# Kernel tuning notes

Measured on AMD Instinct MI355X. Metric: run time of the kernel, lower is better.

## Reference

```python
import jax, jax.numpy as jnp
import numpy as np

BINS = 2048       # self.bins in HistogramQuant
UPSAMPLE = 128    # self.upsample_rate


def setup_inputs() -> dict:
    key = jax.random.key(0)
    k1, k2 = jax.random.split(key)
    x = jax.random.normal(k1, (64, 1024, 1024), dtype=jnp.float32)
    histogram = jax.random.uniform(k2, (BINS,), dtype=jnp.float32)
    min_val = jnp.zeros((1,), dtype=jnp.float32)
    max_val = jnp.ones((1,), dtype=jnp.float32)
    return {"x": x, "histogram": histogram, "min_val": min_val, "max_val": max_val}


def reference(x, histogram, min_val, max_val):
    # Observer-update branch of HistogramQuant.forward (counter > 0, state
    # initialized). Returns concat([new_histogram(2048), new_min, new_max]).
    xs = jax.lax.stop_gradient(x)  # torch: x = x_orig.detach()
    mn = min_val[0]
    mx = max_val[0]
    cur_min = jnp.min(xs)
    cur_max = jnp.max(xs)
    cmin = jnp.minimum(cur_min, mn)
    cmax0 = jnp.maximum(cur_max, mx)

    # _adjust_min_max
    hbw = (mx - mn) / (BINS * UPSAMPLE)  # fine-grained bin width of old hist
    dr_f = jnp.ceil((cmax0 - cmin) / (BINS * hbw))  # downsample_rate
    cmax = cmax0 + (dr_f * (BINS * hbw) - (cmax0 - cmin))
    start_idx = jnp.round((mn - cmin) / hbw).astype(jnp.int32)

    # torch.histc(x, BINS, min=int(cmin), max=int(cmax)) -- truncated range
    hmn = jnp.trunc(cmin)
    hmx = jnp.trunc(cmax)
    rel = (xs - hmn) / (hmx - hmn)
    idx = jnp.clip(jnp.floor(rel * BINS), 0, BINS - 1).astype(jnp.int32)
    in_range = (xs >= hmn) & (xs <= hmx)  # histc ignores out-of-range values
    hist_new = jax.ops.segment_sum(
        in_range.astype(jnp.float32).ravel(), idx.ravel(), num_segments=BINS)

    # _combine_histograms, done analytically: the torch code upsamples the old
    # histogram by UPSAMPLE, places it at start_idx inside a BINS*dr grid,
    # cumsums, and samples every dr-th entry. The cumsum at grid position p
    # equals (with q = p - start_idx) the inclusive prefix sum of the
    # upsampled old histogram at q, which has closed form
    #   pref[q//U] + (q%U + 1) * old_hist[q//U]
    # so we never materialize the BINS*dr or BINS*U arrays.
    dr = dr_f.astype(jnp.int32)
    pref = jnp.concatenate(
        [jnp.zeros((1,), histogram.dtype), jnp.cumsum(histogram)[:-1]]) * UPSAMPLE
    p = (jnp.arange(BINS, dtype=jnp.int32) + 1) * dr - 1  # sampled positions
    q = p - start_idx
    qc = jnp.clip(q, 0, BINS * UPSAMPLE - 1)
    j = qc // UPSAMPLE
    frac = (qc % UPSAMPLE).astype(histogram.dtype)
    integral = jnp.where(q < 0, 0.0, pref[j] + (frac + 1.0) * histogram[j])
    shifted = jnp.concatenate(
        [jnp.zeros((1,), integral.dtype), integral[:-1]])
    interp = (integral - shifted) / UPSAMPLE

    same = (cmin == mn) & (cmax == mx)
    new_hist = hist_new + jnp.where(same, histogram, interp)
    return jnp.concatenate([new_hist, cmin[None], cmax[None]])
```

## Files before the change

kernel.cpp:

```cpp
#include <hip/hip_runtime.h>
#include <math.h>

#define BINS 2048
#define UPSAMPLE 128

__device__ __forceinline__ unsigned enc_f32(float f) {
    unsigned u = __float_as_uint(f);
    return (u & 0x80000000u) ? ~u : (u | 0x80000000u);
}
__device__ __forceinline__ float dec_f32(unsigned e) {
    unsigned u = (e & 0x80000000u) ? (e ^ 0x80000000u) : ~e;
    return __uint_as_float(u);
}

__global__ void hq_init(float* out) {
    int i = blockIdx.x * blockDim.x + threadIdx.x;
    if (i < BINS) out[i] = 0.0f;
    if (i == BINS)     ((unsigned*)out)[BINS]     = 0xFFFFFFFFu;
    if (i == BINS + 1) ((unsigned*)out)[BINS + 1] = 0u;
}

__global__ void __launch_bounds__(256) hq_minmax(const float4* __restrict__ x4, long n4,
                                                 const float* __restrict__ xt, int ntail,
                                                 unsigned* mm) {
    float vmin = INFINITY, vmax = -INFINITY;
    long i0 = (long)blockIdx.x * blockDim.x + threadIdx.x;
    long stride = (long)gridDim.x * blockDim.x;
    for (long i = i0; i < n4; i += stride) {
        float4 v = x4[i];
        vmin = fminf(vmin, fminf(fminf(v.x, v.y), fminf(v.z, v.w)));
        vmax = fmaxf(vmax, fmaxf(fmaxf(v.x, v.y), fmaxf(v.z, v.w)));
    }
    if (blockIdx.x == 0 && threadIdx.x < ntail) {
        float xv = xt[threadIdx.x];
        vmin = fminf(vmin, xv);
        vmax = fmaxf(vmax, xv);
    }
    #pragma unroll
    for (int off = 32; off; off >>= 1) {
        vmin = fminf(vmin, __shfl_xor(vmin, off));
        vmax = fmaxf(vmax, __shfl_xor(vmax, off));
    }
    __shared__ float smin[4], smax[4];
    int wid = threadIdx.x >> 6, lane = threadIdx.x & 63;
    if (lane == 0) { smin[wid] = vmin; smax[wid] = vmax; }
    __syncthreads();
    if (threadIdx.x == 0) {
        float bmin = fminf(fminf(smin[0], smin[1]), fminf(smin[2], smin[3]));
        float bmax = fmaxf(fmaxf(smax[0], smax[1]), fmaxf(smax[2], smax[3]));
        atomicMin(&mm[0], enc_f32(bmin));
        atomicMax(&mm[1], enc_f32(bmax));
    }
}

__device__ __forceinline__ void hist_bin_add(float xv, float hmn, float hmx, float range,
                                             unsigned* sh) {
    if (xv >= hmn && xv <= hmx) {
        float rel = (xv - hmn) / range;
        int idx = (int)fminf(fmaxf(floorf(rel * (float)BINS), 0.0f), (float)(BINS - 1));
        atomicAdd(&sh[idx], 1u);
    }
}

__global__ void __launch_bounds__(1024) hq_hist(const float4* __restrict__ x4, long n4,
                                                const float* __restrict__ xt, int ntail,
                                                float* __restrict__ out,
                                                const float* __restrict__ min_val,
                                                const float* __restrict__ max_val) {
    __shared__ unsigned sh[BINS];
    for (int i = threadIdx.x; i < BINS; i += blockDim.x) sh[i] = 0u;

    const unsigned* mm = (const unsigned*)(out + BINS);
    float mn = min_val[0], mx = max_val[0];
    float cmin  = fminf(dec_f32(mm[0]), mn);
    float cmax0 = fmaxf(dec_f32(mm[1]), mx);
    float hbw = (mx - mn) / (float)(BINS * UPSAMPLE);
    float bw  = (float)BINS * hbw;
    float dr_f = ceilf((cmax0 - cmin) / bw);
    float cmax = cmax0 + (dr_f * bw - (cmax0 - cmin));
    float hmn = truncf(cmin), hmx = truncf(cmax);
    float range = hmx - hmn;
    __syncthreads();

    long i0 = (long)blockIdx.x * blockDim.x + threadIdx.x;
    long stride = (long)gridDim.x * blockDim.x;
    for (long i = i0; i < n4; i += stride) {
        float4 v = x4[i];
        hist_bin_add(v.x, hmn, hmx, range, sh);
        hist_bin_add(v.y, hmn, hmx, range, sh);
        hist_bin_add(v.z, hmn, hmx, range, sh);
        hist_bin_add(v.w, hmn, hmx, range, sh);
    }
    if (blockIdx.x == 0 && threadIdx.x < ntail) {
        hist_bin_add(xt[threadIdx.x], hmn, hmx, range, sh);
    }
    __syncthreads();
    for (int i = threadIdx.x; i < BINS; i += blockDim.x) {
        unsigned c = sh[i];
        if (c) atomicAdd(&out[i], (float)c);
    }
}

__global__ void __launch_bounds__(1024) hq_finalize(float* __restrict__ out,
                                                    const float* __restrict__ old_hist,
                                                    const float* __restrict__ min_val,
                                                    const float* __restrict__ max_val) {
    __shared__ float h[BINS];
    __shared__ float sc[2][BINS];
    int t = threadIdx.x;

    const unsigned* mm = (const unsigned*)(out + BINS);
    unsigned emin = mm[0], emax = mm[1];
    float mn = min_val[0], mx = max_val[0];

    h[t]        = old_hist[t];
    h[t + 1024] = old_hist[t + 1024];
    sc[0][t]        = h[t];
    sc[0][t + 1024] = h[t + 1024];
    __syncthreads();

    int src = 0;
    for (int off = 1; off < BINS; off <<= 1) {
        int dst = src ^ 1;
        #pragma unroll
        for (int k = 0; k < 2; ++k) {
            int i = t + k * 1024;
            float v = sc[src][i];
            if (i >= off) v += sc[src][i - off];
            sc[dst][i] = v;
        }
        __syncthreads();
        src = dst;
    }
    const float* incl = sc[src];

    float cmin  = fminf(dec_f32(emin), mn);
    float cmax0 = fmaxf(dec_f32(emax), mx);
    float hbw = (mx - mn) / (float)(BINS * UPSAMPLE);
    float bw  = (float)BINS * hbw;
    float dr_f = ceilf((cmax0 - cmin) / bw);
    float cmax = cmax0 + (dr_f * bw - (cmax0 - cmin));
    int dr = (int)dr_f;
    int start_idx = (int)rintf((mn - cmin) / hbw);
    bool same = (cmin == mn) && (cmax == mx);

    #pragma unroll
    for (int k = 0; k < 2; ++k) {
        int i = t + k * 1024;
        float integ_i = 0.0f, integ_p = 0.0f;
        {
            int q = (i + 1) * dr - 1 - start_idx;
            if (q >= 0) {
                int qc = min(q, BINS * UPSAMPLE - 1);
                int j = qc >> 7;
                float pref = (j ? incl[j - 1] : 0.0f) * (float)UPSAMPLE;
                integ_i = pref + ((float)(qc & 127) + 1.0f) * h[j];
            }
        }
        if (i > 0) {
            int q = i * dr - 1 - start_idx;
            if (q >= 0) {
                int qc = min(q, BINS * UPSAMPLE - 1);
                int j = qc >> 7;
                float pref = (j ? incl[j - 1] : 0.0f) * (float)UPSAMPLE;
                integ_p = pref + ((float)(qc & 127) + 1.0f) * h[j];
            }
        }
        float interp = (integ_i - integ_p) * (1.0f / (float)UPSAMPLE);
        out[i] = out[i] + (same ? h[i] : interp);
    }
    if (t == 0) {
        out[BINS]     = cmin;
        out[BINS + 1] = cmax;
    }
}

extern "C" void kernel_launch(void* const* d_in, const int* in_sizes, int n_in,
                              void* d_out, int out_size, void* d_ws, size_t ws_size,
                              hipStream_t stream) {
    (void)d_ws; (void)ws_size; (void)n_in; (void)out_size;
    const float* x         = (const float*)d_in[0];
    const float* histogram = (const float*)d_in[1];
    const float* min_val   = (const float*)d_in[2];
    const float* max_val   = (const float*)d_in[3];
    float* out = (float*)d_out;

    long n  = (long)in_sizes[0];
    long n4 = n >> 2;
    int ntail = (int)(n & 3);
    const float* xt = x + (n4 << 2);

    hq_init<<<(BINS + 2 + 255) / 256, 256, 0, stream>>>(out);
    hq_minmax<<<2048, 256, 0, stream>>>((const float4*)x, n4, xt, ntail,
                                        (unsigned*)(out + BINS));
    hq_hist<<<512, 1024, 0, stream>>>((const float4*)x, n4, xt, ntail, out,
                                      min_val, max_val);
    hq_finalize<<<1, 1024, 0, stream>>>(out, histogram, min_val, max_val);
}
```

Baseline: 436.2 us.

## Fuse min/max and histogram into one pass via fine-grained integer-bin histogram

Replaces the two passes over x (min/max, then histogram) with one pass. That pass bins every value into a fixed fine grid of width 1/2048. Because the histc range endpoints are truncated to integers, each output bin covers a whole number of fine cells, so the final histogram can be rebuilt from fine counts once min/max are known. A 16K-entry shared window holds the common range, with global atomics for outliers. Per-block partials are reduced in a separate kernel. This halves reads of the 256MB input but adds a large workspace, a 4M-entry init, partial writeback, and serial summing in finalize proportional to the range.

```diff
diff --git a/kernel.cpp b/kernel.cpp
--- a/kernel.cpp
+++ b/kernel.cpp
@@ -3,6 +3,16 @@
 
 #define BINS 2048
 #define UPSAMPLE 128
+
+#define LWIN 16384
+#define LHALF 8192
+#define WIDE_N 4194304
+#define WIDE_HALF 2097152
+#define NBLK 512
+#define RGROUPS 8
+
+#define MM_OFF   WIDE_N
+#define PART_OFF (WIDE_N + 16)
 
 __device__ __forceinline__ unsigned enc_f32(float f) {
     unsigned u = __float_as_uint(f);
@@ -13,105 +23,99 @@
     return __uint_as_float(u);
 }
 
-__global__ void hq_init(float* out) {
-    int i = blockIdx.x * blockDim.x + threadIdx.x;
-    if (i < BINS) out[i] = 0.0f;
-    if (i == BINS)     ((unsigned*)out)[BINS]     = 0xFFFFFFFFu;
-    if (i == BINS + 1) ((unsigned*)out)[BINS + 1] = 0u;
-}
-
-__global__ void __launch_bounds__(256) hq_minmax(const float4* __restrict__ x4, long n4,
+__global__ void __launch_bounds__(256) hq_init(unsigned* ws) {
+    long i = (long)blockIdx.x * blockDim.x + threadIdx.x;
+    ((uint4*)ws)[i] = make_uint4(0u, 0u, 0u, 0u);
+    if (i == 0) {
+        ws[MM_OFF]     = 0xFFFFFFFFu;
+        ws[MM_OFF + 1] = 0u;
+    }
+}
+
+__device__ __forceinline__ void fine_add(float c, float& vmin, float& vmax,
+                                         unsigned* sh, unsigned* ws) {
+    vmin = fminf(vmin, c);
+    vmax = fmaxf(vmax, c);
+    float t = floorf(c * 2048.0f);
+    t = fminf(fmaxf(t, -2097152.0f), 2097151.0f);
+    int fi = (int)t;
+    int li = fi + LHALF;
+    if ((unsigned)li < (unsigned)LWIN) {
+        atomicAdd(&sh[li], 1u);
+    } else {
+        atomicAdd(&ws[fi + WIDE_HALF], 1u);
+    }
+}
+
+__global__ void __launch_bounds__(1024) hq_pass1(const float4* __restrict__ x4, long n4,
                                                  const float* __restrict__ xt, int ntail,
-                                                 unsigned* mm) {
+                                                 unsigned* __restrict__ ws) {
+    __shared__ unsigned sh[LWIN];
+    __shared__ float smin[16], smax[16];
+    for (int i = threadIdx.x; i < LWIN; i += 1024) sh[i] = 0u;
+    __syncthreads();
+
     float vmin = INFINITY, vmax = -INFINITY;
     long i0 = (long)blockIdx.x * blockDim.x + threadIdx.x;
     long stride = (long)gridDim.x * blockDim.x;
     for (long i = i0; i < n4; i += stride) {
         float4 v = x4[i];
-        vmin = fminf(vmin, fminf(fminf(v.x, v.y), fminf(v.z, v.w)));
-        vmax = fmaxf(vmax, fmaxf(fmaxf(v.x, v.y), fmaxf(v.z, v.w)));
+        fine_add(v.x, vmin, vmax, sh, ws);
+        fine_add(v.y, vmin, vmax, sh, ws);
+        fine_add(v.z, vmin, vmax, sh, ws);
+        fine_add(v.w, vmin, vmax, sh, ws);
     }
     if (blockIdx.x == 0 && threadIdx.x < ntail) {
-        float xv = xt[threadIdx.x];
-        vmin = fminf(vmin, xv);
-        vmax = fmaxf(vmax, xv);
-    }
+        fine_add(xt[threadIdx.x], vmin, vmax, sh, ws);
+    }
+
     #pragma unroll
     for (int off = 32; off; off >>= 1) {
         vmin = fminf(vmin, __shfl_xor(vmin, off));
         vmax = fmaxf(vmax, __shfl_xor(vmax, off));
     }
-    __shared__ float smin[4], smax[4];
     int wid = threadIdx.x >> 6, lane = threadIdx.x & 63;
     if (lane == 0) { smin[wid] = vmin; smax[wid] = vmax; }
     __syncthreads();
+
     if (threadIdx.x == 0) {
-        float bmin = fminf(fminf(smin[0], smin[1]), fminf(smin[2], smin[3]));
-        float bmax = fmaxf(fmaxf(smax[0], smax[1]), fmaxf(smax[2], smax[3]));
-        atomicMin(&mm[0], enc_f32(bmin));
-        atomicMax(&mm[1], enc_f32(bmax));
-    }
-}
-
-__device__ __forceinline__ void hist_bin_add(float xv, float hmn, float hmx, float range,
-                                             unsigned* sh) {
-    if (xv >= hmn && xv <= hmx) {
-        float rel = (xv - hmn) / range;
-        int idx = (int)fminf(fmaxf(floorf(rel * (float)BINS), 0.0f), (float)(BINS - 1));
-        atomicAdd(&sh[idx], 1u);
-    }
-}
-
-__global__ void __launch_bounds__(1024) hq_hist(const float4* __restrict__ x4, long n4,
-                                                const float* __restrict__ xt, int ntail,
-                                                float* __restrict__ out,
-                                                const float* __restrict__ min_val,
-                                                const float* __restrict__ max_val) {
-    __shared__ unsigned sh[BINS];
-    for (int i = threadIdx.x; i < BINS; i += blockDim.x) sh[i] = 0u;
-
-    const unsigned* mm = (const unsigned*)(out + BINS);
-    float mn = min_val[0], mx = max_val[0];
-    float cmin  = fminf(dec_f32(mm[0]), mn);
-    float cmax0 = fmaxf(dec_f32(mm[1]), mx);
-    float hbw = (mx - mn) / (float)(BINS * UPSAMPLE);
-    float bw  = (float)BINS * hbw;
-    float dr_f = ceilf((cmax0 - cmin) / bw);
-    float cmax = cmax0 + (dr_f * bw - (cmax0 - cmin));
-    float hmn = truncf(cmin), hmx = truncf(cmax);
-    float range = hmx - hmn;
-    __syncthreads();
-
-    long i0 = (long)blockIdx.x * blockDim.x + threadIdx.x;
-    long stride = (long)gridDim.x * blockDim.x;
-    for (long i = i0; i < n4; i += stride) {
-        float4 v = x4[i];
-        hist_bin_add(v.x, hmn, hmx, range, sh);
-        hist_bin_add(v.y, hmn, hmx, range, sh);
-        hist_bin_add(v.z, hmn, hmx, range, sh);
-        hist_bin_add(v.w, hmn, hmx, range, sh);
-    }
-    if (blockIdx.x == 0 && threadIdx.x < ntail) {
-        hist_bin_add(xt[threadIdx.x], hmn, hmx, range, sh);
-    }
-    __syncthreads();
-    for (int i = threadIdx.x; i < BINS; i += blockDim.x) {
-        unsigned c = sh[i];
-        if (c) atomicAdd(&out[i], (float)c);
-    }
+        float bmin = INFINITY, bmax = -INFINITY;
+        #pragma unroll
+        for (int w = 0; w < 16; ++w) {
+            bmin = fminf(bmin, smin[w]);
+            bmax = fmaxf(bmax, smax[w]);
+        }
+        atomicMin(&ws[MM_OFF], enc_f32(bmin));
+        atomicMax(&ws[MM_OFF + 1], enc_f32(bmax));
+    }
+
+    unsigned* part = ws + PART_OFF + (size_t)blockIdx.x * LWIN;
+    for (int i = threadIdx.x; i < LWIN; i += 1024) part[i] = sh[i];
+}
+
+__global__ void __launch_bounds__(256) hq_reduce(unsigned* __restrict__ ws) {
+    int c = blockIdx.x & 63;
+    int g = blockIdx.x >> 6;
+    int bin = c * 256 + threadIdx.x;
+    const unsigned* p = ws + PART_OFF + bin + (size_t)g * 64 * LWIN;
+    unsigned s = 0;
+    #pragma unroll 8
+    for (int b = 0; b < 64; ++b) s += p[(size_t)b * LWIN];
+    if (s) atomicAdd(&ws[bin + (WIDE_HALF - LHALF)], s);
 }
 
 __global__ void __launch_bounds__(1024) hq_finalize(float* __restrict__ out,
                                                     const float* __restrict__ old_hist,
                                                     const float* __restrict__ min_val,
-                                                    const float* __restrict__ max_val) {
+                                                    const float* __restrict__ max_val,
+                                                    const unsigned* __restrict__ ws) {
     __shared__ float h[BINS];
     __shared__ float sc[2][BINS];
     int t = threadIdx.x;
 
-    const unsigned* mm = (const unsigned*)(out + BINS);
-    unsigned emin = mm[0], emax = mm[1];
     float mn = min_val[0], mx = max_val[0];
+    float cmin  = fminf(dec_f32(ws[MM_OFF]), mn);
+    float cmax0 = fmaxf(dec_f32(ws[MM_OFF + 1]), mx);
 
     h[t]        = old_hist[t];
     h[t + 1024] = old_hist[t + 1024];
@@ -134,19 +138,32 @@
     }
     const float* incl = sc[src];
 
-    float cmin  = fminf(dec_f32(emin), mn);
-    float cmax0 = fmaxf(dec_f32(emax), mx);
     float hbw = (mx - mn) / (float)(BINS * UPSAMPLE);
     float bw  = (float)BINS * hbw;
     float dr_f = ceilf((cmax0 - cmin) / bw);
     float cmax = cmax0 + (dr_f * bw - (cmax0 - cmin));
+    float hmn = truncf(cmin), hmx = truncf(cmax);
     int dr = (int)dr_f;
     int start_idx = (int)rintf((mn - cmin) / hbw);
     bool same = (cmin == mn) && (cmax == mx);
+    int hmn_i = (int)hmn;
+    int range_i = (int)(hmx - hmn);
 
     #pragma unroll
     for (int k = 0; k < 2; ++k) {
         int i = t + k * 1024;
+
+        float hn = 0.0f;
+        if (range_i > 0) {
+            long fi0 = (long)hmn_i * 2048 + (long)i * range_i + WIDE_HALF;
+            unsigned s = 0;
+            for (int r = 0; r < range_i; ++r) {
+                long fi = fi0 + r;
+                if (fi >= 0 && fi < (long)WIDE_N) s += ws[fi];
+            }
+            hn = (float)s;
+        }
+
         float integ_i = 0.0f, integ_p = 0.0f;
         {
             int q = (i + 1) * dr - 1 - start_idx;
@@ -167,7 +184,7 @@
             }
         }
         float interp = (integ_i - integ_p) * (1.0f / (float)UPSAMPLE);
-        out[i] = out[i] + (same ? h[i] : interp);
+        out[i] = hn + (same ? h[i] : interp);
     }
     if (t == 0) {
         out[BINS]     = cmin;
@@ -178,22 +195,21 @@
 extern "C" void kernel_launch(void* const* d_in, const int* in_sizes, int n_in,
                               void* d_out, int out_size, void* d_ws, size_t ws_size,
                               hipStream_t stream) {
-    (void)d_ws; (void)ws_size; (void)n_in; (void)out_size;
+    (void)n_in; (void)out_size; (void)ws_size;
     const float* x         = (const float*)d_in[0];
     const float* histogram = (const float*)d_in[1];
     const float* min_val   = (const float*)d_in[2];
     const float* max_val   = (const float*)d_in[3];
-    float* out = (float*)d_out;
+    float* out   = (float*)d_out;
+    unsigned* ws = (unsigned*)d_ws;
 
     long n  = (long)in_sizes[0];
     long n4 = n >> 2;
     int ntail = (int)(n & 3);
     const float* xt = x + (n4 << 2);
 
-    hq_init<<<(BINS + 2 + 255) / 256, 256, 0, stream>>>(out);
-    hq_minmax<<<2048, 256, 0, stream>>>((const float4*)x, n4, xt, ntail,
-                                        (unsigned*)(out + BINS));
-    hq_hist<<<512, 1024, 0, stream>>>((const float4*)x, n4, xt, ntail, out,
-                                      min_val, max_val);
-    hq_finalize<<<1, 1024, 0, stream>>>(out, histogram, min_val, max_val);
-}
+    hq_init<<<WIDE_N / 4 / 256, 256, 0, stream>>>(ws);
+    hq_pass1<<<NBLK, 1024, 0, stream>>>((const float4*)x, n4, xt, ntail, ws);
+    hq_reduce<<<64 * RGROUPS, 256, 0, stream>>>(ws);
+    hq_finalize<<<1, 1024, 0, stream>>>(out, histogram, min_val, max_val, ws);
+}
```

Measured after the change: 387.7 us. 1.13x faster.
